# Kernel tuning notes

Measured on AMD Instinct MI355X. Metric: run time of the kernel, lower is better.

Reference implementation:

```python
import jax, jax.numpy as jnp
import numpy as np
from math import gcd

N_SIG = 2097152   # signal length
L_FILT = 129      # FIR taps


def setup_inputs() -> dict:
    key = jax.random.key(0)
    k1, k2 = jax.random.split(key)
    x = jax.random.normal(k1, (N_SIG,), dtype=jnp.float32)
    h = jax.random.normal(k2, (L_FILT,), dtype=jnp.float32)
    return {"x": x, "h": h, "up": 3, "down": 2}


def _get_start_index(length):
    if length <= 2:
        return 0
    return (length - 1) // 2


def reference(x, h, up, down):
    # Reduce rates by gcd, as in the torch module.
    g = gcd(up, down)
    up, down = up // g, down // g
    if up == 1 and down == 1:
        return x
    N = x.shape[0]
    L = h.shape[0]
    # zero-stuff: x_up[::up] = up * x  (gain `up` matches resample_poly)
    x_up = jnp.zeros(up * N, dtype=x.dtype).at[::up].set(up * x)
    # full FIR convolution, then phase-offset strided downsample
    full = jnp.convolve(x_up, h.astype(x.dtype), mode="full")  # [up*N + L - 1]
    start = _get_start_index(L)
    n_out = -(-(N * up) // down)  # ceil(N*up/down)
    return full[start::down][:n_out]
```

## Files before the change

### kernel.cpp

```cpp
#include <hip/hip_runtime.h>


#define N_SIG   2097152
#define L_FILT  129
#define NTAPS   43
#define G       4
#define BLK     256
#define GROUPS_PER_BLK (BLK * G)
#define TILE_Q  2112
#define TILE_P  (TILE_Q + TILE_Q / 8)

template <int U, int R>
__device__ __forceinline__ void do_chunk(const float* __restrict__ xs,
                                         const float* __restrict__ h,
                                         int i0, int tid, float (&acc)[3 * G]) {
    const int D = 45 - (i0 + U - 1);
    const int pb = 9 * tid + 9 * (D >> 3) + R;
    float wz[U + 7];
#pragma unroll
    for (int k = 0; k < U + 7; ++k)
        wz[k] = xs[pb + k + ((R + k) >> 3)];
#pragma unroll
    for (int u = 0; u < U; ++u) {
        const float h0 = h[3 * (i0 + u) + 0];
        const float h1 = h[3 * (i0 + u) + 1];
        const float h2 = h[3 * (i0 + u) + 2];
#pragma unroll
        for (int g = 0; g < G; ++g) {
            const float xa = wz[(U - 1 - u) + 2 * g];
            const float xb = wz[(U - 1 - u) + 2 * g + 1];
            acc[3 * g + 0] += xa * h1;
            acc[3 * g + 1] += xb * h0;
            acc[3 * g + 2] += xb * h2;
        }
    }
}

__global__ __launch_bounds__(BLK, 4) void poly_kernel(
    const float* __restrict__ x, const float* __restrict__ h,
    float* __restrict__ out, int n_out)
{
    __shared__ float xs[TILE_P];

    const int tid = threadIdx.x;
    const int b   = blockIdx.x;

    const int tb = 2 * GROUPS_PER_BLK * b - 24;

    for (int q4 = tid; q4 < TILE_Q / 4; q4 += BLK) {
        const int gx = tb + 4 * q4;
        float4 v;
        if (gx >= 0 && gx + 3 < N_SIG) {
            v = *(const float4*)(x + gx);
        } else {
            v.x = (gx     >= 0 && gx     < N_SIG) ? x[gx]     : 0.0f;
            v.y = (gx + 1 >= 0 && gx + 1 < N_SIG) ? x[gx + 1] : 0.0f;
            v.z = (gx + 2 >= 0 && gx + 2 < N_SIG) ? x[gx + 2] : 0.0f;
            v.w = (gx + 3 >= 0 && gx + 3 < N_SIG) ? x[gx + 3] : 0.0f;
        }
        const int q = 4 * q4;
        const int p = q + (q >> 3);
        xs[p + 0] = v.x; xs[p + 1] = v.y; xs[p + 2] = v.z; xs[p + 3] = v.w;
    }
    __syncthreads();

    float acc[3 * G];
#pragma unroll
    for (int k = 0; k < 3 * G; ++k) acc[k] = 0.0f;

#pragma unroll 1
    for (int i0 = 0; i0 < 40; i0 += 8)
        do_chunk<8, 6>(xs, h, i0, tid, acc);
    do_chunk<3, 3>(xs, h, 40, tid, acc);

    const int ob = 3 * GROUPS_PER_BLK * b + 3 * G * tid;
#pragma unroll
    for (int k = 0; k < 3; ++k) {
        if (ob + 4 * k + 3 < n_out) {
            *(float4*)(out + ob + 4 * k) =
                make_float4(3.0f * acc[4 * k + 0], 3.0f * acc[4 * k + 1],
                            3.0f * acc[4 * k + 2], 3.0f * acc[4 * k + 3]);
        }
    }
}

extern "C" void kernel_launch(void* const* d_in, const int* in_sizes, int n_in,
                              void* d_out, int out_size, void* d_ws, size_t ws_size,
                              hipStream_t stream) {
    const float* x = (const float*)d_in[0];
    const float* h = (const float*)d_in[1];
    float* out = (float*)d_out;
    const int blocks = (out_size + 3 * GROUPS_PER_BLK - 1) / (3 * GROUPS_PER_BLK);
    poly_kernel<<<blocks, BLK, 0, stream>>>(x, h, out, out_size);
}
```

Measured before the change: 70.44 us.

## Halve per-thread outputs, fully unroll taps with double-buffered LDS windows

Each thread now computes 6 outputs instead of 12, so the grid doubles and the per-block shared tile halves. The LDS padding changes from one pad per 8 floats to one per 4 floats, matching the new stride of 5 per thread. The tap loop is fully unrolled with two alternating register windows, so the LDS loads for the next chunk overlap the FMAs of the current one. In exchange each LDS load serves fewer FMAs, the overlapping halo is reloaded more often, and stores shrink from float4 to float2.

```diff
diff --git a/kernel.cpp b/kernel.cpp
--- a/kernel.cpp
+++ b/kernel.cpp
@@ -4,31 +4,35 @@
 #define N_SIG   2097152
 #define L_FILT  129
 #define NTAPS   43
-#define G       4
+#define G       2
 #define BLK     256
 #define GROUPS_PER_BLK (BLK * G)
-#define TILE_Q  2112
-#define TILE_P  (TILE_Q + TILE_Q / 8)
+#define TILE_Q  1072
+#define TILE_P  (TILE_Q + TILE_Q / 4)
 
-template <int U, int R>
-__device__ __forceinline__ void do_chunk(const float* __restrict__ xs,
-                                         const float* __restrict__ h,
-                                         int i0, int tid, float (&acc)[3 * G]) {
-    const int D = 45 - (i0 + U - 1);
-    const int pb = 9 * tid + 9 * (D >> 3) + R;
-    float wz[U + 7];
+template <int U, int I0>
+__device__ __forceinline__ void load_win(const float* __restrict__ xs,
+                                         int tid, float (&wz)[U + 3]) {
+    constexpr int D = 46 - U - I0;
+    constexpr int R = D & 3;
+    const int pb = 5 * tid + D + (D >> 2);
 #pragma unroll
-    for (int k = 0; k < U + 7; ++k)
-        wz[k] = xs[pb + k + ((R + k) >> 3)];
+    for (int k = 0; k < U + 3; ++k)
+        wz[k] = xs[pb + k + ((R + k) >> 2)];
+}
+
+template <int U, int I0>
+__device__ __forceinline__ void fmas(const float* __restrict__ h,
+                                     const float (&wz)[U + 3], float (&acc)[3 * G]) {
 #pragma unroll
     for (int u = 0; u < U; ++u) {
-        const float h0 = h[3 * (i0 + u) + 0];
-        const float h1 = h[3 * (i0 + u) + 1];
-        const float h2 = h[3 * (i0 + u) + 2];
+        const float h0 = h[3 * (I0 + u) + 0];
+        const float h1 = h[3 * (I0 + u) + 1];
+        const float h2 = h[3 * (I0 + u) + 2];
 #pragma unroll
         for (int g = 0; g < G; ++g) {
-            const float xa = wz[(U - 1 - u) + 2 * g];
-            const float xb = wz[(U - 1 - u) + 2 * g + 1];
+            const float xa = wz[U - 1 - u + 2 * g];
+            const float xb = wz[U - u + 2 * g];
             acc[3 * g + 0] += xa * h1;
             acc[3 * g + 1] += xb * h0;
             acc[3 * g + 2] += xb * h2;
@@ -58,8 +62,7 @@
             v.z = (gx + 2 >= 0 && gx + 2 < N_SIG) ? x[gx + 2] : 0.0f;
             v.w = (gx + 3 >= 0 && gx + 3 < N_SIG) ? x[gx + 3] : 0.0f;
         }
-        const int q = 4 * q4;
-        const int p = q + (q >> 3);
+        const int p = 5 * q4;
         xs[p + 0] = v.x; xs[p + 1] = v.y; xs[p + 2] = v.z; xs[p + 3] = v.w;
     }
     __syncthreads();
@@ -68,18 +71,26 @@
 #pragma unroll
     for (int k = 0; k < 3 * G; ++k) acc[k] = 0.0f;
 
-#pragma unroll 1
-    for (int i0 = 0; i0 < 40; i0 += 8)
-        do_chunk<8, 6>(xs, h, i0, tid, acc);
-    do_chunk<3, 3>(xs, h, 40, tid, acc);
+    float w0[11], w1[11], wt[6];
+    load_win<8, 0 >(xs, tid, w0);
+    load_win<8, 8 >(xs, tid, w1);
+    fmas<8, 0 >(h, w0, acc);
+    load_win<8, 16>(xs, tid, w0);
+    fmas<8, 8 >(h, w1, acc);
+    load_win<8, 24>(xs, tid, w1);
+    fmas<8, 16>(h, w0, acc);
+    load_win<8, 32>(xs, tid, w0);
+    fmas<8, 24>(h, w1, acc);
+    load_win<3, 40>(xs, tid, wt);
+    fmas<8, 32>(h, w0, acc);
+    fmas<3, 40>(h, wt, acc);
 
     const int ob = 3 * GROUPS_PER_BLK * b + 3 * G * tid;
 #pragma unroll
     for (int k = 0; k < 3; ++k) {
-        if (ob + 4 * k + 3 < n_out) {
-            *(float4*)(out + ob + 4 * k) =
-                make_float4(3.0f * acc[4 * k + 0], 3.0f * acc[4 * k + 1],
-                            3.0f * acc[4 * k + 2], 3.0f * acc[4 * k + 3]);
+        if (ob + 2 * k + 1 < n_out) {
+            *(float2*)(out + ob + 2 * k) =
+                make_float2(3.0f * acc[2 * k], 3.0f * acc[2 * k + 1]);
         }
     }
 }
```

Measured after the change: 73.56 us. 4.4% more time.
